# Optimization experiments

Measured on AMD Instinct MI355X. Metric: run time of the kernel, lower is better.

The kernel has to match this reference:

```python
import jax, jax.numpy as jnp
import numpy as np

NUM_GRAPHS_N = 64  # number of segments in node_batch
NUM_GRAPHS_L = 64  # number of segments in label_batch


def setup_inputs() -> dict:
    key = jax.random.key(0)
    k1, k2, k3, k4, k5 = jax.random.split(key, 5)
    N, D = 16384, 256
    En, El = 8192, 8192
    h = jax.random.normal(k1, (N, D), dtype=jnp.float32)
    node_edge = jax.random.randint(k2, (2, En), 0, N, dtype=jnp.int64)
    node_batch = jnp.sort(jax.random.randint(k3, (En,), 0, NUM_GRAPHS_N, dtype=jnp.int64))
    label_edge = jax.random.randint(k4, (2, El), 0, N, dtype=jnp.int64)
    label_batch = jnp.sort(jax.random.randint(k5, (El,), 0, NUM_GRAPHS_L, dtype=jnp.int64))
    return {"h": h, "node_edge": node_edge, "node_batch": node_batch,
            "label_edge": label_edge, "label_batch": label_batch}


def _cdist(a, b):
    # Euclidean pairwise distance, grad-safe sqrt.
    sq = (jnp.sum(a * a, -1)[:, None] + jnp.sum(b * b, -1)[None, :]
          - 2.0 * (a @ b.T))
    sq = jnp.maximum(sq, 0.0)
    safe = jnp.where(sq > 0, sq, 1.0)
    return jnp.where(sq > 0, jnp.sqrt(safe), 0.0)


def _seg_max(x, seg, num):  # max over axis 0; empty segments -> 0 like torch_scatter
    m = jax.ops.segment_max(x, seg, num_segments=num)
    return jnp.where(jnp.isfinite(m), m, 0.0)


def _seg_mean(x, seg, num):
    s = jax.ops.segment_sum(x, seg, num_segments=num)
    cnt = jax.ops.segment_sum(jnp.ones((x.shape[0], 1), x.dtype), seg, num_segments=num)
    return s / jnp.maximum(cnt, 1.0)


def reference(h, node_edge, node_batch, label_edge, label_batch):
    ef_n = (h[node_edge[0]] + h[node_edge[1]]) * 0.5   # [En, D]
    ef_l = (h[label_edge[0]] + h[label_edge[1]]) * 0.5  # [El, D]
    M = -_cdist(ef_n, ef_l)                              # [En, El]
    # max over cols by label_batch -> [En, Gl], then mean over rows by node_batch
    out_n = _seg_max(M.T, label_batch, NUM_GRAPHS_L).T   # [En, Gl]
    out_n = _seg_mean(out_n, node_batch, NUM_GRAPHS_N)   # [Gn, Gl]
    # max over rows by node_batch -> [Gn, El], then mean over cols by label_batch
    out_l = _seg_max(M, node_batch, NUM_GRAPHS_N)        # [Gn, El]
    out_l = _seg_mean(out_l.T, label_batch, NUM_GRAPHS_L).T  # [Gn, Gl]
    return (out_n + out_l) * 0.5
```

## Files before the change

kernel.cpp:

```cpp
#include <hip/hip_runtime.h>
#include <hip/hip_bf16.h>
#include <math.h>

#define EN 8192
#define EL 8192
#define D  256
#define NG 64
#define INF_BITS 0x7f800000u

typedef __attribute__((ext_vector_type(8))) short  bf16x8;
typedef __attribute__((ext_vector_type(4))) float  f32x4;

__device__ __forceinline__ unsigned short f2bf(float f) {
    unsigned u = __float_as_uint(f);
    unsigned r = (u + 0x7fffu + ((u >> 16) & 1u)) >> 16;
    return (unsigned short)r;
}

__global__ void prep(const float* __restrict__ h,
                     const int* __restrict__ node_edge,
                     const int* __restrict__ label_edge,
                     unsigned short* __restrict__ efn, float* __restrict__ normN,
                     unsigned short* __restrict__ efl, float* __restrict__ normL,
                     unsigned* __restrict__ inf_buf)
{
    int b = blockIdx.x;
    if (b < 1024) {
        uint4 v = make_uint4(INF_BITS, INF_BITS, INF_BITS, INF_BITS);
        ((uint4*)inf_buf)[b * 256 + threadIdx.x] = v;
        return;
    }
    b -= 1024;
    const int* edges; unsigned short* ef; float* norm;
    if (b < 2048) { edges = node_edge;  ef = efn; norm = normN; }
    else          { b -= 2048; edges = label_edge; ef = efl; norm = normL; }

    int wave = threadIdx.x >> 6;
    int lane = threadIdx.x & 63;
    int e = b * 4 + wave;
    int a  = edges[e];
    int bb = edges[EN + e];
    float4 va = ((const float4*)(h + (size_t)a  * D))[lane];
    float4 vb = ((const float4*)(h + (size_t)bb * D))[lane];
    float4 f;
    f.x = 0.5f * (va.x + vb.x);
    f.y = 0.5f * (va.y + vb.y);
    f.z = 0.5f * (va.z + vb.z);
    f.w = 0.5f * (va.w + vb.w);
    float sq = f.x*f.x + f.y*f.y + f.z*f.z + f.w*f.w;
    ushort4 pk;
    pk.x = f2bf(f.x); pk.y = f2bf(f.y); pk.z = f2bf(f.z); pk.w = f2bf(f.w);
    ((ushort4*)(ef + (size_t)e * D))[lane] = pk;
    #pragma unroll
    for (int off = 1; off < 64; off <<= 1)
        sq += __shfl_xor(sq, off, 64);
    if (lane == 0) norm[e] = sq;
}

__launch_bounds__(512, 4)
__global__ void dist_min(const unsigned short* __restrict__ A,
                         const unsigned short* __restrict__ B,
                         const float* __restrict__ normN,
                         const float* __restrict__ normL,
                         const int* __restrict__ node_batch,
                         const int* __restrict__ label_batch,
                         unsigned* __restrict__ bufN,
                         unsigned* __restrict__ bufL)
{
    __shared__ unsigned short As[2][128 * 64];
    __shared__ unsigned short Bs[2][128 * 64];

    const int tid  = threadIdx.x;
    const int lane = tid & 63;
    const int wave = tid >> 6;
    const int quad = lane >> 4;
    const int lc   = lane & 15;
    const int m0   = blockIdx.y * 128;
    const int n0   = blockIdx.x * 128;
    const int wr   = (wave >> 1) * 32;
    const int wc   = (wave & 1) * 64;

    f32x4 acc[2][4];
    #pragma unroll
    for (int i = 0; i < 2; ++i)
        #pragma unroll
        for (int j = 0; j < 4; ++j) {
            f32x4 z = {0.f, 0.f, 0.f, 0.f};
            acc[i][j] = z;
        }

    auto stage = [&](int buf, int kt) {
        #pragma unroll
        for (int t = 0; t < 2; ++t) {
            int c = t * 512 + tid;
            int row = c >> 3, cc = c & 7;
            int scc = cc ^ (row & 7);
            const unsigned short* gp = A + (size_t)(m0 + row) * D + kt * 64 + scc * 8;
            __builtin_amdgcn_global_load_lds(
                (const __attribute__((address_space(1))) void*)gp,
                (__attribute__((address_space(3))) void*)(As[buf] + c * 8), 16, 0, 0);
        }
        #pragma unroll
        for (int t = 0; t < 2; ++t) {
            int c = t * 512 + tid;
            int row = c >> 3, cc = c & 7;
            int scc = cc ^ (row & 7);
            const unsigned short* gp = B + (size_t)(n0 + row) * D + kt * 64 + scc * 8;
            __builtin_amdgcn_global_load_lds(
                (const __attribute__((address_space(1))) void*)gp,
                (__attribute__((address_space(3))) void*)(Bs[buf] + c * 8), 16, 0, 0);
        }
    };

    stage(0, 0);
    __syncthreads();

    int cur = 0;
    for (int kt = 0; kt < 4; ++kt) {
        if (kt < 3) stage(cur ^ 1, kt + 1);

        #pragma unroll
        for (int kk = 0; kk < 2; ++kk) {
            bf16x8 af[2], bfv[4];
            #pragma unroll
            for (int mi = 0; mi < 2; ++mi)
                af[mi] = *(const bf16x8*)(As[cur] + (wr + mi*16 + lc) * 64
                                             + ((kk*4 + quad) ^ (lc & 7)) * 8);
            #pragma unroll
            for (int ni = 0; ni < 4; ++ni)
                bfv[ni] = *(const bf16x8*)(Bs[cur] + (wc + ni*16 + lc) * 64
                                              + ((kk*4 + quad) ^ (lc & 7)) * 8);
            #pragma unroll
            for (int mi = 0; mi < 2; ++mi)
                #pragma unroll
                for (int ni = 0; ni < 4; ++ni)
                    acc[mi][ni] = __builtin_amdgcn_mfma_f32_16x16x32_bf16(
                        af[mi], bfv[ni], acc[mi][ni], 0, 0, 0);
        }
        __syncthreads();
        cur ^= 1;
    }

    float nb[4]; int gl[4];
    #pragma unroll
    for (int ni = 0; ni < 4; ++ni) {
        int col = n0 + wc + ni*16 + lc;
        nb[ni] = normL[col];
        gl[ni] = label_batch[col];
    }
    float na[8]; int gr[8];
    #pragma unroll
    for (int mi = 0; mi < 2; ++mi)
        #pragma unroll
        for (int r = 0; r < 4; ++r) {
            int row = m0 + wr + mi*16 + quad*4 + r;
            na[mi*4 + r] = normN[row];
            gr[mi*4 + r] = node_batch[row];
        }

    #pragma unroll
    for (int mi = 0; mi < 2; ++mi)
        #pragma unroll
        for (int ni = 0; ni < 4; ++ni)
            #pragma unroll
            for (int r = 0; r < 4; ++r)
                acc[mi][ni][r] = fmaxf(
                    fmaf(-2.0f, acc[mi][ni][r], na[mi*4 + r] + nb[ni]), 0.0f);

    const float FINF = __uint_as_float(INF_BITS);

    int glo = label_batch[n0 + wc], ghi = label_batch[n0 + wc + 63];
    if (glo == ghi) {
        float rm[8];
        #pragma unroll
        for (int mi = 0; mi < 2; ++mi)
            #pragma unroll
            for (int r = 0; r < 4; ++r) {
                float m = fminf(fminf(acc[mi][0][r], acc[mi][1][r]),
                                fminf(acc[mi][2][r], acc[mi][3][r]));
                m = fminf(m, __shfl_xor(m, 1, 64));
                m = fminf(m, __shfl_xor(m, 2, 64));
                m = fminf(m, __shfl_xor(m, 4, 64));
                m = fminf(m, __shfl_xor(m, 8, 64));
                rm[mi*4 + r] = m;
            }
        if (lc == 0) {
            #pragma unroll
            for (int mi = 0; mi < 2; ++mi)
                #pragma unroll
                for (int r = 0; r < 4; ++r) {
                    int row = m0 + wr + mi*16 + quad*4 + r;
                    atomicMin(&bufN[row * NG + glo], __float_as_uint(rm[mi*4 + r]));
                }
        }
    } else {
        for (int g = glo; g <= ghi; ++g) {
            bool s0 = (gl[0] == g), s1 = (gl[1] == g), s2 = (gl[2] == g), s3 = (gl[3] == g);
            float rm[8];
            #pragma unroll
            for (int mi = 0; mi < 2; ++mi)
                #pragma unroll
                for (int r = 0; r < 4; ++r) {
                    float m = s0 ? acc[mi][0][r] : FINF;
                    m = fminf(m, s1 ? acc[mi][1][r] : FINF);
                    m = fminf(m, s2 ? acc[mi][2][r] : FINF);
                    m = fminf(m, s3 ? acc[mi][3][r] : FINF);
                    m = fminf(m, __shfl_xor(m, 1, 64));
                    m = fminf(m, __shfl_xor(m, 2, 64));
                    m = fminf(m, __shfl_xor(m, 4, 64));
                    m = fminf(m, __shfl_xor(m, 8, 64));
                    rm[mi*4 + r] = m;
                }
            if (lc == 0) {
                #pragma unroll
                for (int mi = 0; mi < 2; ++mi)
                    #pragma unroll
                    for (int r = 0; r < 4; ++r) {
                        int row = m0 + wr + mi*16 + quad*4 + r;
                        atomicMin(&bufN[row * NG + g], __float_as_uint(rm[mi*4 + r]));
                    }
            }
        }
    }

    int rlo = node_batch[m0 + wr], rhi = node_batch[m0 + wr + 31];
    if (rlo == rhi) {
        float cm[4];
        #pragma unroll
        for (int ni = 0; ni < 4; ++ni) {
            float m = acc[0][ni][0];
            m = fminf(m, acc[0][ni][1]); m = fminf(m, acc[0][ni][2]);
            m = fminf(m, acc[0][ni][3]); m = fminf(m, acc[1][ni][0]);
            m = fminf(m, acc[1][ni][1]); m = fminf(m, acc[1][ni][2]);
            m = fminf(m, acc[1][ni][3]);
            m = fminf(m, __shfl_xor(m, 16, 64));
            m = fminf(m, __shfl_xor(m, 32, 64));
            cm[ni] = m;
        }
        if (quad == 0) {
            #pragma unroll
            for (int ni = 0; ni < 4; ++ni) {
                int col = n0 + wc + ni*16 + lc;
                atomicMin(&bufL[rlo * EL + col], __float_as_uint(cm[ni]));
            }
        }
    } else {
        for (int g = rlo; g <= rhi; ++g) {
            float cm[4];
            #pragma unroll
            for (int ni = 0; ni < 4; ++ni) {
                float m = FINF;
                #pragma unroll
                for (int mi = 0; mi < 2; ++mi)
                    #pragma unroll
                    for (int r = 0; r < 4; ++r)
                        m = fminf(m, (gr[mi*4 + r] == g) ? acc[mi][ni][r] : FINF);
                m = fminf(m, __shfl_xor(m, 16, 64));
                m = fminf(m, __shfl_xor(m, 32, 64));
                cm[ni] = m;
            }
            if (quad == 0) {
                #pragma unroll
                for (int ni = 0; ni < 4; ++ni) {
                    int col = n0 + wc + ni*16 + lc;
                    atomicMin(&bufL[g * EL + col], __float_as_uint(cm[ni]));
                }
            }
        }
    }
}

__device__ __forceinline__ int lbound(const int* __restrict__ a, int n, int v) {
    int lo = 0, hi = n;
    while (lo < hi) { int mid = (lo + hi) >> 1; if (a[mid] < v) lo = mid + 1; else hi = mid; }
    return lo;
}

__global__ void finalize(const unsigned* __restrict__ bufN,
                         const unsigned* __restrict__ bufL,
                         const int* __restrict__ node_batch,
                         const int* __restrict__ label_batch,
                         float* __restrict__ out)
{
    __shared__ float sN[NG];
    __shared__ float sL[NG];
    int gn  = blockIdx.x;
    int tid = threadIdx.x;
    if (tid < NG) { sN[tid] = 0.0f; sL[tid] = 0.0f; }
    __syncthreads();

    int ns = lbound(node_batch, EN, gn);
    int ne = lbound(node_batch, EN, gn + 1);

    {
        int t = tid & 63, strip = tid >> 6;
        float acc = 0.0f;
        for (int i = ns + strip; i < ne; i += 16) {
            unsigned b = bufN[i * NG + t];
            if (b != INF_BITS) acc -= sqrtf(__uint_as_float(b));
        }
        atomicAdd(&sN[t], acc);
    }

    for (int j = tid; j < EL; j += 1024) {
        unsigned b = bufL[gn * EL + j];
        if (b != INF_BITS) {
            int g = label_batch[j];
            atomicAdd(&sL[g], -sqrtf(__uint_as_float(b)));
        }
    }
    __syncthreads();

    if (tid < NG) {
        int t = tid;
        int cn = ne - ns;
        int ls = lbound(label_batch, EL, t);
        int le = lbound(label_batch, EL, t + 1);
        int cl = le - ls;
        float out_n = sN[t] / (float)(cn > 0 ? cn : 1);
        float out_l = sL[t] / (float)(cl > 0 ? cl : 1);
        out[gn * NG + t] = 0.5f * (out_n + out_l);
    }
}

extern "C" void kernel_launch(void* const* d_in, const int* in_sizes, int n_in,
                              void* d_out, int out_size, void* d_ws, size_t ws_size,
                              hipStream_t stream)
{
    const float* h          = (const float*)d_in[0];
    const int* node_edge    = (const int*)d_in[1];
    const int* node_batch   = (const int*)d_in[2];
    const int* label_edge   = (const int*)d_in[3];
    const int* label_batch  = (const int*)d_in[4];
    float* out = (float*)d_out;

    char* ws = (char*)d_ws;
    unsigned short* efn = (unsigned short*)ws; ws += (size_t)EN * D * 2;
    unsigned short* efl = (unsigned short*)ws; ws += (size_t)EL * D * 2;
    float* normN = (float*)ws;                 ws += (size_t)EN * 4;
    float* normL = (float*)ws;                 ws += (size_t)EL * 4;
    unsigned* bufN = (unsigned*)ws;            ws += (size_t)EN * NG * 4;
    unsigned* bufL = (unsigned*)ws;            ws += (size_t)NG * EL * 4;

    prep<<<5120, 256, 0, stream>>>(h, node_edge, label_edge,
                                   efn, normN, efl, normL, bufN);
    dist_min<<<dim3(EL / 128, EN / 128), 512, 0, stream>>>(
        efn, efl, normN, normL, node_batch, label_batch, bufN, bufL);
    finalize<<<NG, 1024, 0, stream>>>(bufN, bufL, node_batch, label_batch, out);
}
```

Measured before the change: 192.0 us.

## Keep full-K A tile resident in LDS and loop over multiple B tiles per block

Each block now loads its 128x256 A tile once into LDS and iterates over 8 consecutive 128-column B tiles, double-buffering B in 128-wide K chunks. This removes repeated A reloads and the per-tile launch/prologue overhead, and overlaps the epilogue of one output tile with prefetch of the next. The grid shrinks from 4096 to 512 blocks and LDS use grows to 128KB per block, so occupancy drops (launch bounds lowered to 2) and there may be too few blocks to fill all CUs.

```diff
diff --git a/kernel.cpp b/kernel.cpp
--- a/kernel.cpp
+++ b/kernel.cpp
@@ -6,6 +6,7 @@
 #define EL 8192
 #define D  256
 #define NG 64
+#define QTILES 8
 #define INF_BITS 0x7f800000u
 
 typedef __attribute__((ext_vector_type(8))) short  bf16x8;
@@ -57,7 +58,7 @@
     if (lane == 0) norm[e] = sq;
 }
 
-__launch_bounds__(512, 4)
+__launch_bounds__(512, 2)
 __global__ void dist_min(const unsigned short* __restrict__ A,
                          const unsigned short* __restrict__ B,
                          const float* __restrict__ normN,
@@ -67,8 +68,8 @@
                          unsigned* __restrict__ bufN,
                          unsigned* __restrict__ bufL)
 {
-    __shared__ unsigned short As[2][128 * 64];
-    __shared__ unsigned short Bs[2][128 * 64];
+    __shared__ unsigned short As[128 * 256];
+    __shared__ unsigned short Bs[2][128 * 128];
 
     const int tid  = threadIdx.x;
     const int lane = tid & 63;
@@ -76,78 +77,38 @@
     const int quad = lane >> 4;
     const int lc   = lane & 15;
     const int m0   = blockIdx.y * 128;
-    const int n0   = blockIdx.x * 128;
+    const int q    = blockIdx.x;
     const int wr   = (wave >> 1) * 32;
     const int wc   = (wave & 1) * 64;
 
-    f32x4 acc[2][4];
     #pragma unroll
-    for (int i = 0; i < 2; ++i)
-        #pragma unroll
-        for (int j = 0; j < 4; ++j) {
-            f32x4 z = {0.f, 0.f, 0.f, 0.f};
-            acc[i][j] = z;
-        }
-
-    auto stage = [&](int buf, int kt) {
-        #pragma unroll
-        for (int t = 0; t < 2; ++t) {
+    for (int t = 0; t < 8; ++t) {
+        int c = t * 512 + tid;
+        int row = c >> 5, cc = c & 31;
+        int scc = cc ^ (row & 7);
+        const unsigned short* gp = A + (size_t)(m0 + row) * D + scc * 8;
+        __builtin_amdgcn_global_load_lds(
+            (const __attribute__((address_space(1))) void*)gp,
+            (__attribute__((address_space(3))) void*)(As + c * 8), 16, 0, 0);
+    }
+
+    auto stageB = [&](int buf, int ot, int ck) {
+        int n0t = q * (QTILES * 128) + ot * 128;
+        #pragma unroll
+        for (int t = 0; t < 4; ++t) {
             int c = t * 512 + tid;
-            int row = c >> 3, cc = c & 7;
+            int row = c >> 4, cc = c & 15;
             int scc = cc ^ (row & 7);
-            const unsigned short* gp = A + (size_t)(m0 + row) * D + kt * 64 + scc * 8;
-            __builtin_amdgcn_global_load_lds(
-                (const __attribute__((address_space(1))) void*)gp,
-                (__attribute__((address_space(3))) void*)(As[buf] + c * 8), 16, 0, 0);
-        }
-        #pragma unroll
-        for (int t = 0; t < 2; ++t) {
-            int c = t * 512 + tid;
-            int row = c >> 3, cc = c & 7;
-            int scc = cc ^ (row & 7);
-            const unsigned short* gp = B + (size_t)(n0 + row) * D + kt * 64 + scc * 8;
+            const unsigned short* gp =
+                B + (size_t)(n0t + row) * D + ck * 128 + scc * 8;
             __builtin_amdgcn_global_load_lds(
                 (const __attribute__((address_space(1))) void*)gp,
                 (__attribute__((address_space(3))) void*)(Bs[buf] + c * 8), 16, 0, 0);
         }
     };
 
-    stage(0, 0);
-    __syncthreads();
-
-    int cur = 0;
-    for (int kt = 0; kt < 4; ++kt) {
-        if (kt < 3) stage(cur ^ 1, kt + 1);
-
-        #pragma unroll
-        for (int kk = 0; kk < 2; ++kk) {
-            bf16x8 af[2], bfv[4];
-            #pragma unroll
-            for (int mi = 0; mi < 2; ++mi)
-                af[mi] = *(const bf16x8*)(As[cur] + (wr + mi*16 + lc) * 64
-                                             + ((kk*4 + quad) ^ (lc & 7)) * 8);
-            #pragma unroll
-            for (int ni = 0; ni < 4; ++ni)
-                bfv[ni] = *(const bf16x8*)(Bs[cur] + (wc + ni*16 + lc) * 64
-                                              + ((kk*4 + quad) ^ (lc & 7)) * 8);
-            #pragma unroll
-            for (int mi = 0; mi < 2; ++mi)
-                #pragma unroll
-                for (int ni = 0; ni < 4; ++ni)
-                    acc[mi][ni] = __builtin_amdgcn_mfma_f32_16x16x32_bf16(
-                        af[mi], bfv[ni], acc[mi][ni], 0, 0, 0);
-        }
-        __syncthreads();
-        cur ^= 1;
-    }
-
-    float nb[4]; int gl[4];
-    #pragma unroll
-    for (int ni = 0; ni < 4; ++ni) {
-        int col = n0 + wc + ni*16 + lc;
-        nb[ni] = normL[col];
-        gl[ni] = label_batch[col];
-    }
+    stageB(0, 0, 0);
+
     float na[8]; int gr[8];
     #pragma unroll
     for (int mi = 0; mi < 2; ++mi)
@@ -157,54 +118,82 @@
             na[mi*4 + r] = normN[row];
             gr[mi*4 + r] = node_batch[row];
         }
-
-    #pragma unroll
-    for (int mi = 0; mi < 2; ++mi)
-        #pragma unroll
-        for (int ni = 0; ni < 4; ++ni)
-            #pragma unroll
-            for (int r = 0; r < 4; ++r)
-                acc[mi][ni][r] = fmaxf(
-                    fmaf(-2.0f, acc[mi][ni][r], na[mi*4 + r] + nb[ni]), 0.0f);
-
+    const int rlo = node_batch[m0 + wr], rhi = node_batch[m0 + wr + 31];
     const float FINF = __uint_as_float(INF_BITS);
 
-    int glo = label_batch[n0 + wc], ghi = label_batch[n0 + wc + 63];
-    if (glo == ghi) {
-        float rm[8];
+    __syncthreads();
+
+    int buf = 0;
+    for (int ot = 0; ot < QTILES; ++ot) {
+        const int n0t = q * (QTILES * 128) + ot * 128;
+
+        float nb[4]; int gl[4];
+        #pragma unroll
+        for (int ni = 0; ni < 4; ++ni) {
+            int col = n0t + wc + ni*16 + lc;
+            nb[ni] = normL[col];
+            gl[ni] = label_batch[col];
+        }
+        int glo = label_batch[n0t + wc], ghi = label_batch[n0t + wc + 63];
+
+        f32x4 acc[2][4];
+        #pragma unroll
+        for (int i = 0; i < 2; ++i)
+            #pragma unroll
+            for (int j = 0; j < 4; ++j) {
+                f32x4 z = {0.f, 0.f, 0.f, 0.f};
+                acc[i][j] = z;
+            }
+
+        #pragma unroll
+        for (int ck = 0; ck < 2; ++ck) {
+            if (!(ot == QTILES - 1 && ck == 1))
+                stageB(buf ^ 1, ck ? ot + 1 : ot, ck ^ 1);
+
+            #pragma unroll
+            for (int kt2 = 0; kt2 < 2; ++kt2) {
+                #pragma unroll
+                for (int kk = 0; kk < 2; ++kk) {
+                    bf16x8 af[2], bfv[4];
+                    int kg = (ck*2 + kt2)*8 + kk*4 + quad;
+                    int kb = kt2*8 + kk*4 + quad;
+                    #pragma unroll
+                    for (int mi = 0; mi < 2; ++mi)
+                        af[mi] = *(const bf16x8*)(As + (wr + mi*16 + lc) * 256
+                                                     + (kg ^ (lc & 7)) * 8);
+                    #pragma unroll
+                    for (int ni = 0; ni < 4; ++ni)
+                        bfv[ni] = *(const bf16x8*)(Bs[buf] + (wc + ni*16 + lc) * 128
+                                                      + (kb ^ (lc & 7)) * 8);
+                    #pragma unroll
+                    for (int mi = 0; mi < 2; ++mi)
+                        #pragma unroll
+                        for (int ni = 0; ni < 4; ++ni)
+                            acc[mi][ni] = __builtin_amdgcn_mfma_f32_16x16x32_bf16(
+                                af[mi], bfv[ni], acc[mi][ni], 0, 0, 0);
+                }
+            }
+            __syncthreads();
+            buf ^= 1;
+        }
+
         #pragma unroll
         for (int mi = 0; mi < 2; ++mi)
             #pragma unroll
-            for (int r = 0; r < 4; ++r) {
-                float m = fminf(fminf(acc[mi][0][r], acc[mi][1][r]),
-                                fminf(acc[mi][2][r], acc[mi][3][r]));
-                m = fminf(m, __shfl_xor(m, 1, 64));
-                m = fminf(m, __shfl_xor(m, 2, 64));
-                m = fminf(m, __shfl_xor(m, 4, 64));
-                m = fminf(m, __shfl_xor(m, 8, 64));
-                rm[mi*4 + r] = m;
-            }
-        if (lc == 0) {
+            for (int ni = 0; ni < 4; ++ni)
+                #pragma unroll
+                for (int r = 0; r < 4; ++r)
+                    acc[mi][ni][r] = fmaxf(
+                        fmaf(-2.0f, acc[mi][ni][r], na[mi*4 + r] + nb[ni]), 0.0f);
+
+        if (glo == ghi) {
+            float rm[8];
             #pragma unroll
             for (int mi = 0; mi < 2; ++mi)
                 #pragma unroll
                 for (int r = 0; r < 4; ++r) {
-                    int row = m0 + wr + mi*16 + quad*4 + r;
-                    atomicMin(&bufN[row * NG + glo], __float_as_uint(rm[mi*4 + r]));
-                }
-        }
-    } else {
-        for (int g = glo; g <= ghi; ++g) {
-            bool s0 = (gl[0] == g), s1 = (gl[1] == g), s2 = (gl[2] == g), s3 = (gl[3] == g);
-            float rm[8];
-            #pragma unroll
-            for (int mi = 0; mi < 2; ++mi)
-                #pragma unroll
-                for (int r = 0; r < 4; ++r) {
-                    float m = s0 ? acc[mi][0][r] : FINF;
-                    m = fminf(m, s1 ? acc[mi][1][r] : FINF);
-                    m = fminf(m, s2 ? acc[mi][2][r] : FINF);
-                    m = fminf(m, s3 ? acc[mi][3][r] : FINF);
+                    float m = fminf(fminf(acc[mi][0][r], acc[mi][1][r]),
+                                    fminf(acc[mi][2][r], acc[mi][3][r]));
                     m = fminf(m, __shfl_xor(m, 1, 64));
                     m = fminf(m, __shfl_xor(m, 2, 64));
                     m = fminf(m, __shfl_xor(m, 4, 64));
@@ -217,44 +206,49 @@
                     #pragma unroll
                     for (int r = 0; r < 4; ++r) {
                         int row = m0 + wr + mi*16 + quad*4 + r;
-                        atomicMin(&bufN[row * NG + g], __float_as_uint(rm[mi*4 + r]));
+                        atomicMin(&bufN[row * NG + glo], __float_as_uint(rm[mi*4 + r]));
                     }
             }
-        }
-    }
-
-    int rlo = node_batch[m0 + wr], rhi = node_batch[m0 + wr + 31];
-    if (rlo == rhi) {
-        float cm[4];
-        #pragma unroll
-        for (int ni = 0; ni < 4; ++ni) {
-            float m = acc[0][ni][0];
-            m = fminf(m, acc[0][ni][1]); m = fminf(m, acc[0][ni][2]);
-            m = fminf(m, acc[0][ni][3]); m = fminf(m, acc[1][ni][0]);
-            m = fminf(m, acc[1][ni][1]); m = fminf(m, acc[1][ni][2]);
-            m = fminf(m, acc[1][ni][3]);
-            m = fminf(m, __shfl_xor(m, 16, 64));
-            m = fminf(m, __shfl_xor(m, 32, 64));
-            cm[ni] = m;
-        }
-        if (quad == 0) {
+        } else {
+            for (int g = glo; g <= ghi; ++g) {
+                bool s0 = (gl[0] == g), s1 = (gl[1] == g),
+                     s2 = (gl[2] == g), s3 = (gl[3] == g);
+                float rm[8];
+                #pragma unroll
+                for (int mi = 0; mi < 2; ++mi)
+                    #pragma unroll
+                    for (int r = 0; r < 4; ++r) {
+                        float m = s0 ? acc[mi][0][r] : FINF;
+                        m = fminf(m, s1 ? acc[mi][1][r] : FINF);
+                        m = fminf(m, s2 ? acc[mi][2][r] : FINF);
+                        m = fminf(m, s3 ? acc[mi][3][r] : FINF);
+                        m = fminf(m, __shfl_xor(m, 1, 64));
+                        m = fminf(m, __shfl_xor(m, 2, 64));
+                        m = fminf(m, __shfl_xor(m, 4, 64));
+                        m = fminf(m, __shfl_xor(m, 8, 64));
+                        rm[mi*4 + r] = m;
+                    }
+                if (lc == 0) {
+                    #pragma unroll
+                    for (int mi = 0; mi < 2; ++mi)
+                        #pragma unroll
+                        for (int r = 0; r < 4; ++r) {
+                            int row = m0 + wr + mi*16 + quad*4 + r;
+                            atomicMin(&bufN[row * NG + g], __float_as_uint(rm[mi*4 + r]));
+                        }
+                }
+            }
+        }
+
+        if (rlo == rhi) {
+            float cm[4];
             #pragma unroll
             for (int ni = 0; ni < 4; ++ni) {
-                int col = n0 + wc + ni*16 + lc;
-                atomicMin(&bufL[rlo * EL + col], __float_as_uint(cm[ni]));
-            }
-        }
-    } else {
-        for (int g = rlo; g <= rhi; ++g) {
-            float cm[4];
-            #pragma unroll
-            for (int ni = 0; ni < 4; ++ni) {
-                float m = FINF;
-                #pragma unroll
-                for (int mi = 0; mi < 2; ++mi)
-                    #pragma unroll
-                    for (int r = 0; r < 4; ++r)
-                        m = fminf(m, (gr[mi*4 + r] == g) ? acc[mi][ni][r] : FINF);
+                float m = acc[0][ni][0];
+                m = fminf(m, acc[0][ni][1]); m = fminf(m, acc[0][ni][2]);
+                m = fminf(m, acc[0][ni][3]); m = fminf(m, acc[1][ni][0]);
+                m = fminf(m, acc[1][ni][1]); m = fminf(m, acc[1][ni][2]);
+                m = fminf(m, acc[1][ni][3]);
                 m = fminf(m, __shfl_xor(m, 16, 64));
                 m = fminf(m, __shfl_xor(m, 32, 64));
                 cm[ni] = m;
@@ -262,8 +256,31 @@
             if (quad == 0) {
                 #pragma unroll
                 for (int ni = 0; ni < 4; ++ni) {
-                    int col = n0 + wc + ni*16 + lc;
-                    atomicMin(&bufL[g * EL + col], __float_as_uint(cm[ni]));
+                    int col = n0t + wc + ni*16 + lc;
+                    atomicMin(&bufL[rlo * EL + col], __float_as_uint(cm[ni]));
+                }
+            }
+        } else {
+            for (int g = rlo; g <= rhi; ++g) {
+                float cm[4];
+                #pragma unroll
+                for (int ni = 0; ni < 4; ++ni) {
+                    float m = FINF;
+                    #pragma unroll
+                    for (int mi = 0; mi < 2; ++mi)
+                        #pragma unroll
+                        for (int r = 0; r < 4; ++r)
+                            m = fminf(m, (gr[mi*4 + r] == g) ? acc[mi][ni][r] : FINF);
+                    m = fminf(m, __shfl_xor(m, 16, 64));
+                    m = fminf(m, __shfl_xor(m, 32, 64));
+                    cm[ni] = m;
+                }
+                if (quad == 0) {
+                    #pragma unroll
+                    for (int ni = 0; ni < 4; ++ni) {
+                        int col = n0t + wc + ni*16 + lc;
+                        atomicMin(&bufL[g * EL + col], __float_as_uint(cm[ni]));
+                    }
                 }
             }
         }
@@ -344,7 +361,7 @@
 
     prep<<<5120, 256, 0, stream>>>(h, node_edge, label_edge,
                                    efn, normN, efl, normL, bufN);
-    dist_min<<<dim3(EL / 128, EN / 128), 512, 0, stream>>>(
+    dist_min<<<dim3(QTILES, EN / 128), 512, 0, stream>>>(
         efn, efl, normN, normL, node_batch, label_batch, bufN, bufL);
     finalize<<<NG, 1024, 0, stream>>>(bufN, bufL, node_batch, label_batch, out);
 }
```

Measured after the change: 188.3 us. Within noise of the previous version (-1.9%).
